# Performance work log

Measured on AMD Instinct MI355X. Metric: run time of the kernel, lower is better.

## Reference

```python
import jax, jax.numpy as jnp
import numpy as np

CHUNK = 128  # intra-chunk causal block size for the chunked linear-attention scan


def setup_inputs() -> dict:
    key = jax.random.key(0)
    ks = jax.random.split(key, 7)
    B, H, N, D, F = 1, 24, 4096, 128, 256
    q = jax.random.normal(ks[0], (B, H, N, D), dtype=jnp.float32)
    k = jax.random.normal(ks[1], (B, H, N, D), dtype=jnp.float32)
    v = jax.random.normal(ks[2], (B, H, N, D), dtype=jnp.float32)
    # fan-in scaling so phi features / accumulated state stay numerically sane
    w1 = jax.random.normal(ks[3], (F, D), dtype=jnp.float32) * (D ** -0.5)
    b1 = jax.random.normal(ks[4], (F,), dtype=jnp.float32) * 0.02
    w2 = jax.random.normal(ks[5], (F, F), dtype=jnp.float32) * (F ** -0.5)
    b2 = jax.random.normal(ks[6], (F,), dtype=jnp.float32) * 0.02
    return {"q": q, "k": k, "v": v, "w1": w1, "b1": b1, "w2": w2, "b2": b2}


def _phi(x, w1, b1, w2, b2):
    # Linear(D->F) -> SiLU -> Linear(F->F)
    h = jax.nn.silu(jnp.einsum('bnd,fd->bnf', x, w1) + b1)
    return jnp.einsum('bnf,gf->bng', h, w2) + b2


def _causal_scan(qp, kp, vf):
    # out_t = q_t . (sum_{s<=t} k_s v_s^T) / (t+1), chunked parallel form.
    BH, N, F = qp.shape
    D = vf.shape[-1]
    C = CHUNK
    nC = N // C
    qc = qp.reshape(BH, nC, C, F).transpose(1, 0, 2, 3)  # [nC,BH,C,F]
    kc = kp.reshape(BH, nC, C, F).transpose(1, 0, 2, 3)
    vc = vf.reshape(BH, nC, C, D).transpose(1, 0, 2, 3)
    offsets = (jnp.arange(nC) * C).astype(qp.dtype)
    mask = jnp.tril(jnp.ones((C, C), dtype=qp.dtype))  # include diagonal
    pos = jnp.arange(1, C + 1, dtype=qp.dtype)

    def step(w, inp):
        qb, kb, vb, off = inp
        inter = jnp.einsum('bcf,bfd->bcd', qb, w)
        attn = jnp.einsum('bcf,bsf->bcs', qb, kb) * mask
        intra = jnp.einsum('bcs,bsd->bcd', attn, vb)
        counts = off + pos  # global (token_idx + 1)
        out = (inter + intra) / counts[None, :, None]
        w = w + jnp.einsum('bcf,bcd->bfd', kb, vb)
        return w, out

    w0 = jnp.zeros((BH, F, D), dtype=qp.dtype)
    _, outs = jax.lax.scan(step, w0, (qc, kc, vc, offsets))  # outs [nC,BH,C,D]
    return outs.transpose(1, 0, 2, 3).reshape(BH, N, D)


def reference(q, k, v, w1, b1, w2, b2):
    B, H, N, D = q.shape
    qf = q.reshape(B * H, N, D)
    kf = k.reshape(B * H, N, D)
    vf = v.reshape(B * H, N, D)
    qp = _phi(qf, w1, b1, w2, b2)
    kp = _phi(kf, w1, b1, w2, b2)
    out_fwd = _causal_scan(qp, kp, vf)
    out_rev = _causal_scan(qp[:, ::-1], kp[:, ::-1], vf[:, ::-1])[:, ::-1]
    return (out_fwd + out_rev).reshape(B, H, N, D)
```

## Files before the change

### kernel.cpp

```cpp
#include <hip/hip_runtime.h>


typedef __attribute__((ext_vector_type(8))) _Float16 f16x8;
typedef __attribute__((ext_vector_type(4))) _Float16 f16x4;
typedef __attribute__((ext_vector_type(4))) float f32x4;

#define MFMA16(a, b, c) __builtin_amdgcn_mfma_f32_16x16x32_f16((a), (b), (c), 0, 0, 0)

constexpr int BH   = 24;
constexpr int NSEQ = 4096;
constexpr int DD   = 128;
constexpr int FF   = 256;
constexpr int CHK  = 128;
constexpr int NC   = NSEQ / CHK;
constexpr int NROWS = BH * NSEQ;

__global__ void prep_kernel(const float* __restrict__ w1, const float* __restrict__ w2,
                            _Float16* __restrict__ w1h, _Float16* __restrict__ w2h) {
  int i = blockIdx.x * 256 + threadIdx.x;
  if (i < FF * DD) w1h[i] = (_Float16)w1[i];
  if (i < FF * FF) w2h[i] = (_Float16)w2[i];
}

__global__ void vt_kernel(const float* __restrict__ v, _Float16* __restrict__ vT) {
  __shared__ __align__(16) _Float16 lt[128][136];
  int blk = blockIdx.x;
  int c = blk & 31, bh = blk >> 5;
  const float* vc = v + ((size_t)bh * NSEQ + c * CHK) * DD;
  int tid = threadIdx.x;
#pragma unroll
  for (int it = 0; it < 16; ++it) {
    int flat = it * 1024 + tid * 4;
    int s = flat >> 7, d0 = flat & 127;
    float4 xv = *(const float4*)&vc[(size_t)s * DD + d0];
    lt[d0 + 0][s] = (_Float16)xv.x;
    lt[d0 + 1][s] = (_Float16)xv.y;
    lt[d0 + 2][s] = (_Float16)xv.z;
    lt[d0 + 3][s] = (_Float16)xv.w;
  }
  __syncthreads();
#pragma unroll
  for (int it = 0; it < 8; ++it) {
    int flat = it * 256 + tid;
    int d = flat >> 4, sg = flat & 15;
    *(f16x8*)&vT[((size_t)bh * DD + d) * NSEQ + c * CHK + sg * 8] =
        *(const f16x8*)&lt[d][sg * 8];
  }
}

__global__ __launch_bounds__(1024, 4)
void phi_kernel(const float* __restrict__ q, const float* __restrict__ k,
                const float* __restrict__ b1, const float* __restrict__ b2,
                const _Float16* __restrict__ w1h, const _Float16* __restrict__ w2h,
                _Float16* __restrict__ qp, _Float16* __restrict__ kp,
                _Float16* __restrict__ kpT) {
  __shared__ __align__(16) char smem[137216];
  _Float16 (*xs)[136]  = (_Float16(*)[136])smem;
  _Float16 (*w1s)[136] = (_Float16(*)[136])(smem + 34816);
  _Float16 (*hs)[264]  = (_Float16(*)[264])smem;
  _Float16 (*w2s)[136] = (_Float16(*)[136])(smem + 67584);
  _Float16 (*os)[264]  = (_Float16(*)[264])smem;
  _Float16 (*ot)[136]  = (_Float16(*)[136])(smem + 67584);
  int blk = blockIdx.x;
  const float* src;
  _Float16* dst;
  bool isk;
  int rb;
  if (blk < NROWS / 128) { src = q; dst = qp; rb = blk * 128; isk = false; }
  else                   { src = k; dst = kp; rb = (blk - NROWS / 128) * 128; isk = true; }
  int tid = threadIdx.x;
  int lane = tid & 63, wv = tid >> 6, lr = lane & 15, lq = lane >> 4;
  int wm = wv & 3, wn = wv >> 2;

  f16x8 p0r[4], p1r[4];
#pragma unroll
  for (int it = 0; it < 4; ++it) {
    int flat = it * 1024 + tid;
    int g = flat >> 4, cg = flat & 15;
    p0r[it] = *(const f16x8*)&w2h[(size_t)g * FF + cg * 8];
    p1r[it] = *(const f16x8*)&w2h[(size_t)g * FF + 128 + cg * 8];
  }
#pragma unroll
  for (int it = 0; it < 4; ++it) {
    int flat = it * 1024 + tid;
    int f = flat >> 4, cg = flat & 15;
    *(f16x8*)&w1s[f][cg * 8] = *(const f16x8*)&w1h[f * DD + cg * 8];
  }
#pragma unroll
  for (int it = 0; it < 4; ++it) {
    int flat = it * 1024 + tid;
    int r = flat >> 5, dg = flat & 31;
    float4 xv = *(const float4*)&src[(size_t)(rb + r) * DD + dg * 4];
    f16x4 hv = {(_Float16)xv.x, (_Float16)xv.y, (_Float16)xv.z, (_Float16)xv.w};
    *(f16x4*)&xs[r][dg * 4] = hv;
  }
  __syncthreads();

  f32x4 acc[2][4] = {};
#pragma unroll
  for (int ks = 0; ks < 4; ++ks) {
    f16x8 av[2];
#pragma unroll
    for (int im = 0; im < 2; ++im)
      av[im] = *(const f16x8*)&xs[wm * 32 + im * 16 + lr][ks * 32 + lq * 8];
#pragma unroll
    for (int fn = 0; fn < 4; ++fn) {
      f16x8 bv = *(const f16x8*)&w1s[wn * 64 + fn * 16 + lr][ks * 32 + lq * 8];
#pragma unroll
      for (int im = 0; im < 2; ++im) acc[im][fn] = MFMA16(av[im], bv, acc[im][fn]);
    }
  }
  __syncthreads();

#pragma unroll
  for (int it = 0; it < 4; ++it) {
    int flat = it * 1024 + tid;
    int g = flat >> 4, cg = flat & 15;
    *(f16x8*)&w2s[g][cg * 8] = p0r[it];
  }
#pragma unroll
  for (int im = 0; im < 2; ++im)
#pragma unroll
    for (int fn = 0; fn < 4; ++fn) {
      int f = wn * 64 + fn * 16 + lr;
      float bb = b1[f];
      int r0 = wm * 32 + im * 16 + lq * 4;
#pragma unroll
      for (int r = 0; r < 4; ++r) {
        float xv = acc[im][fn][r] + bb;
        hs[r0 + r][f] = (_Float16)(xv / (1.0f + __expf(-xv)));
      }
    }
  __syncthreads();

  f32x4 ac2[2][4] = {};
#pragma unroll
  for (int ks = 0; ks < 4; ++ks) {
    f16x8 av[2];
#pragma unroll
    for (int im = 0; im < 2; ++im)
      av[im] = *(const f16x8*)&hs[wm * 32 + im * 16 + lr][ks * 32 + lq * 8];
#pragma unroll
    for (int fn = 0; fn < 4; ++fn) {
      f16x8 bv = *(const f16x8*)&w2s[wn * 64 + fn * 16 + lr][ks * 32 + lq * 8];
#pragma unroll
      for (int im = 0; im < 2; ++im) ac2[im][fn] = MFMA16(av[im], bv, ac2[im][fn]);
    }
  }
  __syncthreads();
#pragma unroll
  for (int it = 0; it < 4; ++it) {
    int flat = it * 1024 + tid;
    int g = flat >> 4, cg = flat & 15;
    *(f16x8*)&w2s[g][cg * 8] = p1r[it];
  }
  __syncthreads();
#pragma unroll
  for (int ks = 0; ks < 4; ++ks) {
    f16x8 av[2];
#pragma unroll
    for (int im = 0; im < 2; ++im)
      av[im] = *(const f16x8*)&hs[wm * 32 + im * 16 + lr][128 + ks * 32 + lq * 8];
#pragma unroll
    for (int fn = 0; fn < 4; ++fn) {
      f16x8 bv = *(const f16x8*)&w2s[wn * 64 + fn * 16 + lr][ks * 32 + lq * 8];
#pragma unroll
      for (int im = 0; im < 2; ++im) ac2[im][fn] = MFMA16(av[im], bv, ac2[im][fn]);
    }
  }
  __syncthreads();

  int bh = rb >> 12, s0 = rb & 4095;
#pragma unroll
  for (int im = 0; im < 2; ++im)
#pragma unroll
    for (int fn = 0; fn < 4; ++fn) {
      int g = wn * 64 + fn * 16 + lr;
      float bb = b2[g];
      int r0 = wm * 32 + im * 16 + lq * 4;
#pragma unroll
      for (int r = 0; r < 4; ++r) {
        _Float16 val = (_Float16)(ac2[im][fn][r] + bb);
        os[r0 + r][g] = val;
        if (isk) ot[g][r0 + r] = val;
      }
    }
  __syncthreads();
#pragma unroll
  for (int it = 0; it < 4; ++it) {
    int flat = it * 1024 + tid;
    int r = flat >> 5, cg = flat & 31;
    *(f16x8*)&dst[(size_t)(rb + r) * FF + cg * 8] = *(const f16x8*)&os[r][cg * 8];
  }
  if (isk) {
#pragma unroll
    for (int it = 0; it < 4; ++it) {
      int flat = it * 1024 + tid;
      int f = flat >> 4, sg = flat & 15;
      *(f16x8*)&kpT[((size_t)bh * FF + f) * NSEQ + s0 + sg * 8] = *(const f16x8*)&ot[f][sg * 8];
    }
  }
}

__global__ __launch_bounds__(512, 2)
void s_kernel(const _Float16* __restrict__ vT, const _Float16* __restrict__ kpT,
              _Float16* __restrict__ S) {
  __shared__ __align__(16) _Float16 vt[128][136];
  __shared__ __align__(16) _Float16 kt[256][136];
  int blk = blockIdx.x;
  int c = blk & 31, bh = blk >> 5;
  int tid = threadIdx.x;
#pragma unroll
  for (int it = 0; it < 4; ++it) {
    int flat = it * 512 + tid;
    int d = flat >> 4, sg = flat & 15;
    *(f16x8*)&vt[d][sg * 8] = *(const f16x8*)&vT[((size_t)bh * DD + d) * NSEQ + c * CHK + sg * 8];
  }
#pragma unroll
  for (int it = 0; it < 8; ++it) {
    int flat = it * 512 + tid;
    int f = flat >> 4, sg = flat & 15;
    *(f16x8*)&kt[f][sg * 8] = *(const f16x8*)&kpT[((size_t)bh * FF + f) * NSEQ + c * CHK + sg * 8];
  }
  __syncthreads();
  int lane = tid & 63, wv = tid >> 6, lr = lane & 15, lq = lane >> 4;
  int wmd = wv & 1, wnf = wv >> 1;
  f32x4 acc[4][4] = {};
#pragma unroll
  for (int ks = 0; ks < 4; ++ks) {
    f16x8 av[4];
#pragma unroll
    for (int im = 0; im < 4; ++im)
      av[im] = *(const f16x8*)&vt[wmd * 64 + im * 16 + lr][ks * 32 + lq * 8];
#pragma unroll
    for (int fn = 0; fn < 4; ++fn) {
      f16x8 bv = *(const f16x8*)&kt[wnf * 64 + fn * 16 + lr][ks * 32 + lq * 8];
#pragma unroll
      for (int im = 0; im < 4; ++im) acc[im][fn] = MFMA16(av[im], bv, acc[im][fn]);
    }
  }
  _Float16* Sp = S + ((size_t)bh * NC + c) * (size_t)(DD * FF);
#pragma unroll
  for (int im = 0; im < 4; ++im)
#pragma unroll
    for (int fn = 0; fn < 4; ++fn) {
      int f = wnf * 64 + fn * 16 + lr;
#pragma unroll
      for (int r = 0; r < 4; ++r) {
        int d = wmd * 64 + im * 16 + lq * 4 + r;
        Sp[(size_t)d * FF + f] = (_Float16)acc[im][fn][r];
      }
    }
}

__global__ void prefix_kernel(_Float16* S_Wr, _Float16* __restrict__ Wf) {
  size_t idx = (size_t)blockIdx.x * 256 + threadIdx.x;
  int bh = (int)(idx >> 15);
  int df = (int)(idx & 32767);
  size_t base = (size_t)bh * NC * 32768 + df;
  float vals[NC];
#pragma unroll
  for (int c = 0; c < NC; ++c) vals[c] = (float)S_Wr[base + (size_t)c * 32768];
  float run = 0.f;
#pragma unroll
  for (int c = 0; c < NC; ++c) { Wf[base + (size_t)c * 32768] = (_Float16)run; run += vals[c]; }
  run = 0.f;
#pragma unroll
  for (int c = NC - 1; c >= 0; --c) { S_Wr[base + (size_t)c * 32768] = (_Float16)run; run += vals[c]; }
}

__global__ __launch_bounds__(512, 2)
void scan_kernel(const _Float16* __restrict__ qp, const _Float16* __restrict__ kp,
                 const _Float16* __restrict__ vT, const _Float16* __restrict__ Wf,
                 const _Float16* __restrict__ Wr, float* __restrict__ out) {
  __shared__ __align__(16) _Float16 vt[128][136];
  __shared__ __align__(16) _Float16 P[128][136];
  int blk = blockIdx.x;
  int c = blk & 31, bh = blk >> 5;
  const _Float16* qpc = qp + ((size_t)bh * NSEQ + c * CHK) * FF;
  const _Float16* kpc = kp + ((size_t)bh * NSEQ + c * CHK) * FF;
  int tid = threadIdx.x, lane = tid & 63, wv = tid >> 6, lr = lane & 15, lq = lane >> 4;
  int wm = wv & 3, wn = wv >> 2;

  f16x8 aq[2][8];
#pragma unroll
  for (int im = 0; im < 2; ++im)
#pragma unroll
    for (int ks = 0; ks < 8; ++ks)
      aq[im][ks] = *(const f16x8*)&qpc[(size_t)(wm * 32 + im * 16 + lr) * FF + ks * 32 + lq * 8];
#pragma unroll
  for (int it = 0; it < 4; ++it) {
    int flat = it * 512 + tid;
    int d = flat >> 4, sg = flat & 15;
    *(f16x8*)&vt[d][sg * 8] = *(const f16x8*)&vT[((size_t)bh * DD + d) * NSEQ + c * CHK + sg * 8];
  }
  f16x8 bk[2][8];
#pragma unroll
  for (int ks = 0; ks < 8; ++ks)
    bk[0][ks] = *(const f16x8*)&kpc[(size_t)(wn * 64 + lr) * FF + ks * 32 + lq * 8];
  f32x4 pacc[2][4] = {};
#pragma unroll
  for (int j = 0; j < 4; ++j) {
    int cur = j & 1;
    if (j < 3)
#pragma unroll
      for (int ks = 0; ks < 8; ++ks)
        bk[cur ^ 1][ks] = *(const f16x8*)&kpc[(size_t)(wn * 64 + (j + 1) * 16 + lr) * FF + ks * 32 + lq * 8];
#pragma unroll
    for (int ks = 0; ks < 8; ++ks)
#pragma unroll
      for (int im = 0; im < 2; ++im)
        pacc[im][j] = MFMA16(aq[im][ks], bk[cur][ks], pacc[im][j]);
  }
#pragma unroll
  for (int im = 0; im < 2; ++im)
#pragma unroll
    for (int j = 0; j < 4; ++j)
#pragma unroll
      for (int r = 0; r < 4; ++r)
        P[wm * 32 + im * 16 + lq * 4 + r][wn * 64 + j * 16 + lr] = (_Float16)pacc[im][j][r];

  const _Float16* Wfc = Wf + ((size_t)bh * NC + c) * (size_t)(DD * FF);
  const _Float16* Wrc = Wr + ((size_t)bh * NC + c) * (size_t)(DD * FF);
  f16x8 bf[8], br[8];
#pragma unroll
  for (int ks = 0; ks < 8; ++ks) {
    int d = wn * 64 + lr;
    bf[ks] = *(const f16x8*)&Wfc[(size_t)d * FF + ks * 32 + lq * 8];
    br[ks] = *(const f16x8*)&Wrc[(size_t)d * FF + ks * 32 + lq * 8];
  }
  __syncthreads();

  f32x4 af[2][4] = {}, ar[2][4] = {};
#pragma unroll
  for (int jd = 0; jd < 4; ++jd) {
#pragma unroll
    for (int ks = 0; ks < 8; ++ks)
#pragma unroll
      for (int im = 0; im < 2; ++im) {
        af[im][jd] = MFMA16(aq[im][ks], bf[ks], af[im][jd]);
        ar[im][jd] = MFMA16(aq[im][ks], br[ks], ar[im][jd]);
      }
    if (jd < 3)
#pragma unroll
      for (int ks = 0; ks < 8; ++ks) {
        int d = wn * 64 + (jd + 1) * 16 + lr;
        bf[ks] = *(const f16x8*)&Wfc[(size_t)d * FF + ks * 32 + lq * 8];
        br[ks] = *(const f16x8*)&Wrc[(size_t)d * FF + ks * 32 + lq * 8];
      }
    {
      int ks = jd;
      f16x8 bv[4];
#pragma unroll
      for (int jd2 = 0; jd2 < 4; ++jd2)
        bv[jd2] = *(const f16x8*)&vt[wn * 64 + jd2 * 16 + lr][ks * 32 + lq * 8];
#pragma unroll
      for (int im = 0; im < 2; ++im) {
        int irow = wm * 32 + im * 16 + lr;
        f16x8 p = *(const f16x8*)&P[irow][ks * 32 + lq * 8];
        f16x8 pf = p, pr = p;
#pragma unroll
        for (int jj = 0; jj < 8; ++jj) {
          int s = ks * 32 + lq * 8 + jj;
          pf[jj] = (s <= irow) ? p[jj] : (_Float16)0.0f;
          pr[jj] = (s >= irow) ? p[jj] : (_Float16)0.0f;
        }
#pragma unroll
        for (int jd2 = 0; jd2 < 4; ++jd2) {
          af[im][jd2] = MFMA16(pf, bv[jd2], af[im][jd2]);
          ar[im][jd2] = MFMA16(pr, bv[jd2], ar[im][jd2]);
        }
      }
    }
  }

  float* oc = out + ((size_t)bh * NSEQ + c * CHK) * DD;
#pragma unroll
  for (int im = 0; im < 2; ++im)
#pragma unroll
    for (int jd = 0; jd < 4; ++jd) {
      int d = wn * 64 + jd * 16 + lr;
#pragma unroll
      for (int r = 0; r < 4; ++r) {
        int il = wm * 32 + im * 16 + lq * 4 + r;
        int gi = c * CHK + il;
        oc[(size_t)il * DD + d] = af[im][jd][r] / (float)(gi + 1) + ar[im][jd][r] / (float)(NSEQ - gi);
      }
    }
}

extern "C" void kernel_launch(void* const* d_in, const int* in_sizes, int n_in,
                              void* d_out, int out_size, void* d_ws, size_t ws_size,
                              hipStream_t stream) {
  const float* q  = (const float*)d_in[0];
  const float* k  = (const float*)d_in[1];
  const float* v  = (const float*)d_in[2];
  const float* w1 = (const float*)d_in[3];
  const float* b1 = (const float*)d_in[4];
  const float* w2 = (const float*)d_in[5];
  const float* b2 = (const float*)d_in[6];
  float* out = (float*)d_out;

  char* ws = (char*)d_ws;
  const size_t SZ = 50331648ull;
  _Float16* w1h = (_Float16*)(ws);
  _Float16* w2h = (_Float16*)(ws + 65536);
  _Float16* qp  = (_Float16*)(ws + 196608);
  _Float16* kp  = (_Float16*)(ws + 196608 + SZ);
  _Float16* kpT = (_Float16*)(ws + 196608 + 2 * SZ);
  _Float16* S   = (_Float16*)(ws + 196608 + 3 * SZ);
  _Float16* vT  = (_Float16*)(ws + 196608 + 4 * SZ);
  _Float16* Wf  = kpT;
  _Float16* Wr  = S;

  prep_kernel<<<dim3(256), dim3(256), 0, stream>>>(w1, w2, w1h, w2h);
  vt_kernel<<<dim3(BH * NC), dim3(256), 0, stream>>>(v, vT);
  phi_kernel<<<dim3(2 * NROWS / 128), dim3(1024), 0, stream>>>(q, k, b1, b2, w1h, w2h, qp, kp, kpT);
  s_kernel<<<dim3(BH * NC), dim3(512), 0, stream>>>(vT, kpT, S);
  prefix_kernel<<<dim3(BH * DD * FF / 256), dim3(256), 0, stream>>>(S, Wf);
  scan_kernel<<<dim3(BH * NC), dim3(512), 0, stream>>>(qp, kp, vT, Wf, Wr, out);
}
```

Baseline: 405.1 us.

## Shrink phi kernel tiles and read MLP weights directly from global

```diff
diff --git a/kernel.cpp b/kernel.cpp
--- a/kernel.cpp
+++ b/kernel.cpp
@@ -48,47 +48,31 @@
   }
 }
 
-__global__ __launch_bounds__(1024, 4)
+__global__ __launch_bounds__(512, 8)
 void phi_kernel(const float* __restrict__ q, const float* __restrict__ k,
                 const float* __restrict__ b1, const float* __restrict__ b2,
                 const _Float16* __restrict__ w1h, const _Float16* __restrict__ w2h,
                 _Float16* __restrict__ qp, _Float16* __restrict__ kp,
                 _Float16* __restrict__ kpT) {
-  __shared__ __align__(16) char smem[137216];
-  _Float16 (*xs)[136]  = (_Float16(*)[136])smem;
-  _Float16 (*w1s)[136] = (_Float16(*)[136])(smem + 34816);
-  _Float16 (*hs)[264]  = (_Float16(*)[264])smem;
-  _Float16 (*w2s)[136] = (_Float16(*)[136])(smem + 67584);
-  _Float16 (*os)[264]  = (_Float16(*)[264])smem;
-  _Float16 (*ot)[136]  = (_Float16(*)[136])(smem + 67584);
+  __shared__ __align__(16) char smem[34816];
+  _Float16 (*xs)[136] = (_Float16(*)[136])smem;
+  _Float16 (*hs)[264] = (_Float16(*)[264])smem;
+  _Float16 (*os)[264] = (_Float16(*)[264])smem;
+  _Float16 (*ot)[68]  = (_Float16(*)[68])smem;
   int blk = blockIdx.x;
   const float* src;
   _Float16* dst;
-  bool isk;
-  int rb;
-  if (blk < NROWS / 128) { src = q; dst = qp; rb = blk * 128; isk = false; }
-  else                   { src = k; dst = kp; rb = (blk - NROWS / 128) * 128; isk = true; }
+  bool isk = (blk & 1);
+  int rb = (blk >> 1) * 64;
+  if (!isk) { src = q; dst = qp; }
+  else      { src = k; dst = kp; }
   int tid = threadIdx.x;
   int lane = tid & 63, wv = tid >> 6, lr = lane & 15, lq = lane >> 4;
-  int wm = wv & 3, wn = wv >> 2;
-
-  f16x8 p0r[4], p1r[4];
+  int wm = wv & 1, wn = wv >> 1;
+
 #pragma unroll
   for (int it = 0; it < 4; ++it) {
-    int flat = it * 1024 + tid;
-    int g = flat >> 4, cg = flat & 15;
-    p0r[it] = *(const f16x8*)&w2h[(size_t)g * FF + cg * 8];
-    p1r[it] = *(const f16x8*)&w2h[(size_t)g * FF + 128 + cg * 8];
-  }
-#pragma unroll
-  for (int it = 0; it < 4; ++it) {
-    int flat = it * 1024 + tid;
-    int f = flat >> 4, cg = flat & 15;
-    *(f16x8*)&w1s[f][cg * 8] = *(const f16x8*)&w1h[f * DD + cg * 8];
-  }
-#pragma unroll
-  for (int it = 0; it < 4; ++it) {
-    int flat = it * 1024 + tid;
+    int flat = it * 512 + tid;
     int r = flat >> 5, dg = flat & 31;
     float4 xv = *(const float4*)&src[(size_t)(rb + r) * DD + dg * 4];
     f16x4 hv = {(_Float16)xv.x, (_Float16)xv.y, (_Float16)xv.z, (_Float16)xv.w};
@@ -99,25 +83,21 @@
   f32x4 acc[2][4] = {};
 #pragma unroll
   for (int ks = 0; ks < 4; ++ks) {
+    f16x8 bv[4];
+#pragma unroll
+    for (int fn = 0; fn < 4; ++fn)
+      bv[fn] = *(const f16x8*)&w1h[(size_t)(wn * 64 + fn * 16 + lr) * DD + ks * 32 + lq * 8];
     f16x8 av[2];
 #pragma unroll
     for (int im = 0; im < 2; ++im)
       av[im] = *(const f16x8*)&xs[wm * 32 + im * 16 + lr][ks * 32 + lq * 8];
 #pragma unroll
-    for (int fn = 0; fn < 4; ++fn) {
-      f16x8 bv = *(const f16x8*)&w1s[wn * 64 + fn * 16 + lr][ks * 32 + lq * 8];
-#pragma unroll
-      for (int im = 0; im < 2; ++im) acc[im][fn] = MFMA16(av[im], bv, acc[im][fn]);
-    }
-  }
-  __syncthreads();
-
-#pragma unroll
-  for (int it = 0; it < 4; ++it) {
-    int flat = it * 1024 + tid;
-    int g = flat >> 4, cg = flat & 15;
-    *(f16x8*)&w2s[g][cg * 8] = p0r[it];
-  }
+    for (int fn = 0; fn < 4; ++fn)
+#pragma unroll
+      for (int im = 0; im < 2; ++im) acc[im][fn] = MFMA16(av[im], bv[fn], acc[im][fn]);
+  }
+  __syncthreads();
+
 #pragma unroll
   for (int im = 0; im < 2; ++im)
 #pragma unroll
@@ -128,45 +108,26 @@
 #pragma unroll
       for (int r = 0; r < 4; ++r) {
         float xv = acc[im][fn][r] + bb;
-        hs[r0 + r][f] = (_Float16)(xv / (1.0f + __expf(-xv)));
+        hs[r0 + r][f] = (_Float16)(xv * __builtin_amdgcn_rcpf(1.0f + __expf(-xv)));
       }
     }
   __syncthreads();
 
   f32x4 ac2[2][4] = {};
 #pragma unroll
-  for (int ks = 0; ks < 4; ++ks) {
+  for (int ks = 0; ks < 8; ++ks) {
+    f16x8 bv[4];
+#pragma unroll
+    for (int fn = 0; fn < 4; ++fn)
+      bv[fn] = *(const f16x8*)&w2h[(size_t)(wn * 64 + fn * 16 + lr) * FF + ks * 32 + lq * 8];
     f16x8 av[2];
 #pragma unroll
     for (int im = 0; im < 2; ++im)
       av[im] = *(const f16x8*)&hs[wm * 32 + im * 16 + lr][ks * 32 + lq * 8];
 #pragma unroll
-    for (int fn = 0; fn < 4; ++fn) {
-      f16x8 bv = *(const f16x8*)&w2s[wn * 64 + fn * 16 + lr][ks * 32 + lq * 8];
-#pragma unroll
-      for (int im = 0; im < 2; ++im) ac2[im][fn] = MFMA16(av[im], bv, ac2[im][fn]);
-    }
-  }
-  __syncthreads();
-#pragma unroll
-  for (int it = 0; it < 4; ++it) {
-    int flat = it * 1024 + tid;
-    int g = flat >> 4, cg = flat & 15;
-    *(f16x8*)&w2s[g][cg * 8] = p1r[it];
-  }
-  __syncthreads();
-#pragma unroll
-  for (int ks = 0; ks < 4; ++ks) {
-    f16x8 av[2];
-#pragma unroll
-    for (int im = 0; im < 2; ++im)
-      av[im] = *(const f16x8*)&hs[wm * 32 + im * 16 + lr][128 + ks * 32 + lq * 8];
-#pragma unroll
-    for (int fn = 0; fn < 4; ++fn) {
-      f16x8 bv = *(const f16x8*)&w2s[wn * 64 + fn * 16 + lr][ks * 32 + lq * 8];
-#pragma unroll
-      for (int im = 0; im < 2; ++im) ac2[im][fn] = MFMA16(av[im], bv, ac2[im][fn]);
-    }
+    for (int fn = 0; fn < 4; ++fn)
+#pragma unroll
+      for (int im = 0; im < 2; ++im) ac2[im][fn] = MFMA16(av[im], bv[fn], ac2[im][fn]);
   }
   __syncthreads();
 
@@ -179,24 +140,35 @@
       float bb = b2[g];
       int r0 = wm * 32 + im * 16 + lq * 4;
 #pragma unroll
-      for (int r = 0; r < 4; ++r) {
-        _Float16 val = (_Float16)(ac2[im][fn][r] + bb);
-        os[r0 + r][g] = val;
-        if (isk) ot[g][r0 + r] = val;
-      }
+      for (int r = 0; r < 4; ++r)
+        os[r0 + r][g] = (_Float16)(ac2[im][fn][r] + bb);
     }
   __syncthreads();
 #pragma unroll
   for (int it = 0; it < 4; ++it) {
-    int flat = it * 1024 + tid;
+    int flat = it * 512 + tid;
     int r = flat >> 5, cg = flat & 31;
     *(f16x8*)&dst[(size_t)(rb + r) * FF + cg * 8] = *(const f16x8*)&os[r][cg * 8];
   }
+
   if (isk) {
+    __syncthreads();
+#pragma unroll
+    for (int im = 0; im < 2; ++im)
+#pragma unroll
+      for (int fn = 0; fn < 4; ++fn) {
+        int g = wn * 64 + fn * 16 + lr;
+        float bb = b2[g];
+        int r0 = wm * 32 + im * 16 + lq * 4;
+#pragma unroll
+        for (int r = 0; r < 4; ++r)
+          ot[g][r0 + r] = (_Float16)(ac2[im][fn][r] + bb);
+      }
+    __syncthreads();
 #pragma unroll
     for (int it = 0; it < 4; ++it) {
-      int flat = it * 1024 + tid;
-      int f = flat >> 4, sg = flat & 15;
+      int flat = it * 512 + tid;
+      int f = flat >> 3, sg = flat & 7;
       *(f16x8*)&kpT[((size_t)bh * FF + f) * NSEQ + s0 + sg * 8] = *(const f16x8*)&ot[f][sg * 8];
     }
   }
@@ -415,7 +387,7 @@
 
   prep_kernel<<<dim3(256), dim3(256), 0, stream>>>(w1, w2, w1h, w2h);
   vt_kernel<<<dim3(BH * NC), dim3(256), 0, stream>>>(v, vT);
-  phi_kernel<<<dim3(2 * NROWS / 128), dim3(1024), 0, stream>>>(q, k, b1, b2, w1h, w2h, qp, kp, kpT);
+  phi_kernel<<<dim3(2 * NROWS / 64), dim3(512), 0, stream>>>(q, k, b1, b2, w1h, w2h, qp, kp, kpT);
   s_kernel<<<dim3(BH * NC), dim3(512), 0, stream>>>(vT, kpT, S);
   prefix_kernel<<<dim3(BH * DD * FF / 256), dim3(256), 0, stream>>>(S, Wf);
   scan_kernel<<<dim3(BH * NC), dim3(512), 0, stream>>>(qp, kp, vT, Wf, Wr, out);
```

Measured after the change: 478.1 us. +18.0%, slower.
